# Kernel tuning notes

Hardware: AMD Instinct MI355X
Metric: run time of the kernel (lower is better)

## Reference

```python
import jax, jax.numpy as jnp
import numpy as np

# ---- fixed architecture constants (from init_kwargs) ----
N_WALL, N_ROOF, N_WINDOW = 4, 1, 2
N_RC = N_WALL + N_ROOF
HID = 32
ENC_LEN = 48
DT = 900.0
R_OPAQUE, C_OPAQUE = 10.0, 1.0e5
R_TRANS = 2.0
DIRECT_COEF, ABS_WALL_COEF, ABS_ROOF_COEF = 0.5, 0.5, 0.5
C_ZONE = 1.0e5
B, T = 2048, 1440


def setup_inputs() -> dict:
    key = jax.random.key(0)
    k0, k1, k2 = jax.random.split(key, 3)
    input_X = jax.random.normal(k0, (B, T, 7), dtype=jnp.float32)
    # EnvelopeRC deterministic inits
    rc_R_inv = jnp.concatenate([
        1.0 / (10.0 + 1.0 * jnp.arange(N_WALL, dtype=jnp.float32)),
        1.0 / (20.0 + 2.0 * jnp.arange(N_ROOF, dtype=jnp.float32))])
    rc_C_inv = jnp.concatenate([
        1.0 / (80.0 + 10.0 * jnp.arange(N_WALL, dtype=jnp.float32)),
        1.0 / (60.0 + 10.0 * jnp.arange(N_ROOF, dtype=jnp.float32))])
    window_R_inv = 1.0 / (1.0 + 0.1 * jnp.arange(N_WINDOW, dtype=jnp.float32))
    # Internal MLP: xavier_uniform with gain 0.1, zero bias
    lim1 = 0.1 * np.sqrt(6.0 / (2 + HID))
    int_W1 = jax.random.uniform(k1, (HID, 2), jnp.float32, -lim1, lim1)
    int_b1 = jnp.zeros((HID,), jnp.float32)
    lim2 = 0.1 * np.sqrt(6.0 / (HID + 1))
    int_W2 = jax.random.uniform(k2, (1, HID), jnp.float32, -lim2, lim2)
    int_b2 = jnp.zeros((1,), jnp.float32)
    return {
        'input_X': input_X,
        'rc_R_inv': rc_R_inv, 'rc_C_inv': rc_C_inv, 'window_R_inv': window_R_inv,
        'hvac_gain': jnp.float32(0.1),
        'int_W1': int_W1, 'int_b1': int_b1, 'int_W2': int_W2, 'int_b2': int_b2,
        'int_gain': jnp.float32(0.1),
        'direct_gain': jnp.float32(0.1), 'abs_wall': jnp.float32(0.1), 'abs_roof': jnp.float32(0.1),
        'zone_C_inv': jnp.float32(1.0 / 10000.0),
    }


def _forward(input_X, rc_R_inv, rc_C_inv, window_R_inv, hvac_gain,
             int_W1, int_b1, int_W2, int_b2, int_gain,
             direct_gain, abs_wall, abs_roof, zone_C_inv):
    sp = jax.nn.softplus
    Bn, Tn = input_X.shape[0], input_X.shape[1]
    tz_gt  = input_X[:, :, 0]   # [B,T]
    t_amb  = input_X[:, :, 1]
    sol    = input_X[:, :, 2]
    int_x  = input_X[:, :, 3:6]
    hvac_x = input_X[:, :, 6]

    # Internal MLP (state-free -> vectorized over time)
    h1  = jax.nn.relu(jnp.einsum('bti,hi->bth', int_x[:, :, :2], int_W1) + int_b1)
    sch = jax.nn.sigmoid(jnp.einsum('bth,oh->bto', h1, int_W2) + int_b2)[:, :, 0] + int_x[:, :, 2]
    q_int  = sp(int_gain) * 0.1 * sch          # [B,T]
    q_hvac = sp(hvac_gain) * 0.1 * hvac_x      # [B,T]

    # Bounded RC parameters
    r_inv   = sp(rc_R_inv) * (1.0 / R_OPAQUE)  # [n_rc]
    c_inv   = sp(rc_C_inv) * (1.0 / C_OPAQUE)  # [n_rc]
    win_rsum = jnp.sum(sp(window_R_inv)) * (1.0 / R_TRANS)
    abs_rc  = jnp.where(jnp.arange(N_RC) < N_WALL,
                        sp(abs_wall) * ABS_WALL_COEF,
                        sp(abs_roof) * ABS_ROOF_COEF)   # [n_rc]
    q_dir   = sp(direct_gain) * DIRECT_COEF * sol       # [B,T]
    cz_inv  = sp(zone_C_inv) * (1.0 / C_ZONE)

    # Initial state: Tmid_i = 0.7*Tzone0 + 0.3*Tamb0
    Tz0   = tz_gt[:, 0]                                      # [B]
    Tmid0 = jnp.broadcast_to((0.7 * Tz0 + 0.3 * t_amb[:, 0])[:, None], (Bn, N_RC))

    # Teacher forcing during encoder window: carry GT zone temp while t+1 < enc_len
    tz_gt_next = jnp.concatenate([tz_gt[:, 1:], tz_gt[:, -1:]], axis=1)  # [B,T]
    use_gt = (jnp.arange(Tn) + 1) < ENC_LEN                              # [T]

    xs = (t_amb.T, sol.T, q_dir.T, q_int.T, q_hvac.T, tz_gt_next.T, use_gt)

    def step(carry, x):
        Tz, Tmid = carry                      # [B], [B,n_rc]
        ta, so, qd, qi, qh, gt_next, ug = x
        q_in  = (ta[:, None] - Tmid) * r_inv
        q_out = (Tmid - Tz[:, None]) * r_inv
        dTmid = (q_in - q_out + so[:, None] * abs_rc) * c_inv
        q_env = jnp.sum(q_out, axis=1) + (ta - Tz) * win_rsum
        dTz   = (q_env + qi + qh + qd) * cz_inv
        Tz_new   = Tz + dTz * DT
        Tmid_new = Tmid + dTmid * DT
        Tz_carry = jnp.where(ug, gt_next, Tz_new)
        return (Tz_carry, Tmid_new), Tz_new

    _, tz_seq = jax.lax.scan(step, (Tz0, Tmid0), xs)   # [T,B]
    return jnp.transpose(tz_seq)[:, :, None]           # [B,T,1]


def reference(input_X, rc_R_inv, rc_C_inv, window_R_inv, hvac_gain,
              int_W1, int_b1, int_W2, int_b2, int_gain,
              direct_gain, abs_wall, abs_roof, zone_C_inv):
    return _forward(input_X, rc_R_inv, rc_C_inv, window_R_inv, hvac_gain,
                    int_W1, int_b1, int_W2, int_b2, int_gain,
                    direct_gain, abs_wall, abs_roof, zone_C_inv)
```

## Files before the change

kernel.cpp:

```cpp
#include <hip/hip_runtime.h>
#include <math.h>

#define BATCH 2048
#define TLEN  1440
#define CL0   48
#define CLS   12
#define NS    116
#define NCC   117
#define ER    128
#define TB    64
#define TT    48
#define LP    65

#define E_OFF    0
#define XC_OFF   (E_OFF + BATCH*ER*8)
#define A12_OFF  (XC_OFF + BATCH*NCC*8)
#define VCOL_OFF (A12_OFF + 64)
#define PRM_OFF  (VCOL_OFF + 96)
#define WS_FLOATS (PRM_OFF + 32)

__device__ __forceinline__ float sp_precise(float x) { return log1pf(expf(x)); }

__global__ void k0_params(const float* __restrict__ rcR, const float* __restrict__ rcC,
                          const float* __restrict__ winR, const float* __restrict__ hvg,
                          const float* __restrict__ ing, const float* __restrict__ dg,
                          const float* __restrict__ aw, const float* __restrict__ ar,
                          const float* __restrict__ zc, float* __restrict__ ws) {
  __shared__ float A0s[36], Ma[36], Mb[36], A4s[36], vbuf[2][8];
  int ln = threadIdx.x;
  float r[5], cc[5];
  #pragma unroll
  for (int j = 0; j < 5; ++j) { r[j] = sp_precise(rcR[j]) * 0.1f; cc[j] = sp_precise(rcC[j]) * 1e-5f; }
  float w    = (sp_precise(winR[0]) + sp_precise(winR[1])) * 0.5f;
  float cz   = sp_precise(zc[0]) * 1e-5f;
  float aW   = sp_precise(aw[0]) * 0.5f, aR = sp_precise(ar[0]) * 0.5f;
  float dtcz = 900.f * cz;
  if (ln == 0) {
    float* prm = ws + PRM_OFF;
    float rsum = 0.f;
    for (int j = 0; j < 5; ++j) {
      float P = 900.f * r[j] * cc[j];
      prm[j]      = P;
      prm[5 + j]  = 1.f - 2.f * P;
      prm[10 + j] = 900.f * cc[j] * ((j < 4) ? aW : aR);
      prm[15 + j] = dtcz * r[j];
      rsum += r[j];
    }
    prm[20] = 1.f - dtcz * (w + rsum);
    prm[21] = dtcz * w;
    prm[22] = dtcz;
    prm[23] = sp_precise(ing[0]) * 0.1f;
    prm[24] = sp_precise(hvg[0]) * 0.1f;
    prm[25] = sp_precise(dg[0])  * 0.5f;
    for (int i = 0; i < 36; ++i) A0s[i] = 0.f;
    A0s[0] = prm[20];
    for (int j = 0; j < 5; ++j) {
      A0s[0 * 6 + 1 + j]       = dtcz * r[j];
      A0s[(1 + j) * 6 + 0]     = prm[j];
      A0s[(1 + j) * 6 + 1 + j] = prm[5 + j];
    }
  }
  __syncthreads();
  int i6 = ln / 6, j6 = ln % 6;
  bool act = ln < 36;
#define MM(DST, L, R) { if (act) { float s = 0.f; \
  for (int m = 0; m < 6; ++m) s = fmaf((L)[i6 * 6 + m], (R)[m * 6 + j6], s); \
  (DST)[ln] = s; } __syncthreads(); }
  MM(Mb, A0s, A0s);
  MM(Ma, Mb, Mb);
  if (act) A4s[ln] = Ma[ln];
  __syncthreads();
  MM(Mb, Ma, Ma);
  MM(Ma, Mb, A4s);
  if (act) ws[A12_OFF + ln] = Ma[ln];
  if (ln < 6) vbuf[0][ln] = A0s[ln];
  __syncthreads();
  int cur = 0;
  for (int k = 0; k < CLS; ++k) {
    if (ln < 6) {
      ws[VCOL_OFF + ln * CLS + k] = vbuf[cur][ln];
      float s = 0.f;
      for (int m = 0; m < 6; ++m) s = fmaf(vbuf[cur][m], A0s[m * 6 + ln], s);
      vbuf[1 - cur][ln] = s;
    }
    __syncthreads();
    cur ^= 1;
  }
}

__global__ __launch_bounds__(256) void k2a_scan(const float* __restrict__ X,
    const float* __restrict__ W1, const float* __restrict__ B1,
    const float* __restrict__ W2, const float* __restrict__ B2,
    float* __restrict__ out, float* __restrict__ ws) {
  __shared__ float sTa[TT * LP], sSo[TT * LP], sU[TT * LP], sTz[TT * LP];
  int tile   = blockIdx.x;
  int tile_t = tile >> 5;
  int tile_b = tile & 31;
  int t0 = tile_t * TT, b0 = tile_b * TB;
  const float* prm = ws + PRM_OFF;
  float P0 = prm[0], P1 = prm[1], P2 = prm[2], P3 = prm[3], P4 = prm[4];
  float M0 = prm[5], M1 = prm[6], M2 = prm[7], M3 = prm[8], M4 = prm[9];
  float Q0 = prm[10], Q1 = prm[11], Q2 = prm[12], Q3 = prm[13], Q4 = prm[14];
  float K0 = prm[15], K1 = prm[16], K2 = prm[17], K3 = prm[18], K4 = prm[19];
  float AZ = prm[20];
  float dtczw = prm[21], dtcz = prm[22], cInt = prm[23], cHv = prm[24], cDir = prm[25];
  float b2v = B2[0];

  #pragma unroll 4
  for (int r = 0; r < (TB * TT) / 256; ++r) {
    int e  = threadIdx.x + 256 * r;
    int bl = e / TT;
    int tt = e - bl * TT;
    const float* x = X + ((size_t)(b0 + bl) * TLEN + (t0 + tt)) * 7;
    float x0 = x[0], ta = x[1], so = x[2], x3 = x[3], x4 = x[4], x5 = x[5], hv = x[6];
    float acc = b2v;
    #pragma unroll
    for (int h = 0; h < 32; ++h) {
      float z = fmaf(W1[2 * h], x3, fmaf(W1[2 * h + 1], x4, B1[h]));
      acc = fmaf(W2[h], fmaxf(z, 0.f), acc);
    }
    float sch = __frcp_rn(1.f + __expf(-acc)) + x5;
    float q = fmaf(cInt, sch, fmaf(cHv, hv, cDir * so));
    float u = fmaf(dtczw, ta, dtcz * q);
    sTa[tt * LP + bl] = ta;
    sSo[tt * LP + bl] = so;
    sU [tt * LP + bl] = u;
    sTz[tt * LP + bl] = x0;
  }
  __syncthreads();

  int w = threadIdx.x >> 6, l = threadIdx.x & 63;
  int b = b0 + l;
  bool tile0 = (tile_t == 0);
  int c, kbeg, ksteps;
  if (tile0) { c = 0; kbeg = 0; ksteps = (w == 0) ? CL0 : 0; }
  else       { c = 1 + (tile_t - 1) * 4 + w; kbeg = w * CLS; ksteps = CLS; }
  float Tz = 0.f, T0 = 0.f, T1 = 0.f, T2 = 0.f, T3 = 0.f, T4 = 0.f;
  if (tile0) {
    float tz0 = sTz[l], ta0 = sTa[l];
    Tz = tz0;
    float tm = fmaf(0.7f, tz0, 0.3f * ta0);
    T0 = T1 = T2 = T3 = T4 = tm;
  }
  for (int k = kbeg; k < kbeg + ksteps; ++k) {
    float ta = sTa[k * LP + l], so = sSo[k * LP + l], u = sU[k * LP + l];
    float d = fmaf(K0, T0, u);
    d = fmaf(K1, T1, d); d = fmaf(K2, T2, d); d = fmaf(K3, T3, d); d = fmaf(K4, T4, d);
    float tzn = fmaf(AZ, Tz, d);
    T0 = fmaf(M0, T0, fmaf(P0, Tz, fmaf(P0, ta, Q0 * so)));
    T1 = fmaf(M1, T1, fmaf(P1, Tz, fmaf(P1, ta, Q1 * so)));
    T2 = fmaf(M2, T2, fmaf(P2, Tz, fmaf(P2, ta, Q2 * so)));
    T3 = fmaf(M3, T3, fmaf(P3, Tz, fmaf(P3, ta, Q3 * so)));
    T4 = fmaf(M4, T4, fmaf(P4, Tz, fmaf(P4, ta, Q4 * so)));
    float nz = tzn;
    if (tile0 && k < 47) nz = sTz[(k + 1) * LP + l];
    sTz[k * LP + l] = tzn;
    Tz = nz;
  }
  if (ksteps > 0) {
    float* ep = ws + E_OFF + ((size_t)b * ER + c) * 8;
    *(float4*)ep       = make_float4(Tz, T0, T1, T2);
    *(float2*)(ep + 4) = make_float2(T3, T4);
  }
  __syncthreads();

  #pragma unroll
  for (int r = 0; r < 3; ++r) {
    int f  = threadIdx.x + 256 * r;
    int bl = f / 12, t4 = f - bl * 12;
    float4 v = make_float4(sTz[(4 * t4 + 0) * LP + bl], sTz[(4 * t4 + 1) * LP + bl],
                           sTz[(4 * t4 + 2) * LP + bl], sTz[(4 * t4 + 3) * LP + bl]);
    *(float4*)(out + (size_t)(b0 + bl) * TLEN + t0 + 4 * t4) = v;
  }
}

__global__ __launch_bounds__(256) void k2s_combine(const float* __restrict__ e,
                                                   float* __restrict__ xc,
                                                   const float* __restrict__ A12) {
  __shared__ float sAp[7][40];
  int ln = threadIdx.x;
  if (ln < 36) sAp[0][ln] = A12[ln];
  __syncthreads();
  int i6 = ln / 6, j6 = ln % 6;
  bool act = ln < 36;
  for (int k = 1; k < 7; ++k) {
    if (act) {
      float s = 0.f;
      #pragma unroll
      for (int m = 0; m < 6; ++m) s = fmaf(sAp[k - 1][i6 * 6 + m], sAp[k - 1][m * 6 + j6], s);
      sAp[k][ln] = s;
    }
    __syncthreads();
  }
  int w = ln >> 6, l = ln & 63;
  int b = blockIdx.x * 4 + w;
  const float* pA = e + ((size_t)b * ER + l) * 8;
  const float* pB = e + ((size_t)b * ER + 64 + l) * 8;
  float yA[6], yB[6];
  { float4 q = *(const float4*)pA; float2 r = *(const float2*)(pA + 4);
    yA[0] = q.x; yA[1] = q.y; yA[2] = q.z; yA[3] = q.w; yA[4] = r.x; yA[5] = r.y; }
  { float4 q = *(const float4*)pB; float2 r = *(const float2*)(pB + 4);
    yB[0] = q.x; yB[1] = q.y; yB[2] = q.z; yB[3] = q.w; yB[4] = r.x; yB[5] = r.y; }
  #pragma unroll
  for (int k = 0; k < 6; ++k) {
    int d = 1 << k;
    int src = (l - d) & 63;
    float tA[6], tB[6];
    #pragma unroll
    for (int j = 0; j < 6; ++j) { tA[j] = __shfl(yA[j], src); tB[j] = __shfl(yB[j], src); }
    bool up = (l >= d);
    float sA[6], sB[6];
    #pragma unroll
    for (int j = 0; j < 6; ++j) { sA[j] = up ? tA[j] : 0.f; sB[j] = up ? tB[j] : tA[j]; }
    float nA[6], nB[6];
    #pragma unroll
    for (int i = 0; i < 6; ++i) {
      float uA = yA[i], uB = yB[i];
      #pragma unroll
      for (int m = 0; m < 6; ++m) {
        float a = sAp[k][i * 6 + m];
        uA = fmaf(a, sA[m], uA);
        uB = fmaf(a, sB[m], uB);
      }
      nA[i] = uA; nB[i] = uB;
    }
    #pragma unroll
    for (int i = 0; i < 6; ++i) { yA[i] = nA[i]; yB[i] = nB[i]; }
  }
  #pragma unroll
  for (int i = 0; i < 6; ++i) {
    float uB = yB[i];
    #pragma unroll
    for (int m = 0; m < 6; ++m) uB = fmaf(sAp[6][i * 6 + m], yA[m], uB);
    yB[i] = uB;
  }
  {
    float* xp = xc + ((size_t)b * NCC + (l + 1)) * 8;
    *(float4*)xp       = make_float4(yA[0], yA[1], yA[2], yA[3]);
    *(float2*)(xp + 4) = make_float2(yA[4], yA[5]);
  }
  if (l < 52) {
    float* xp = xc + ((size_t)b * NCC + (65 + l)) * 8;
    *(float4*)xp       = make_float4(yB[0], yB[1], yB[2], yB[3]);
    *(float2*)(xp + 4) = make_float2(yB[4], yB[5]);
  }
}

__global__ __launch_bounds__(256) void k2c_correct(float* __restrict__ out,
                                                   const float* __restrict__ ws) {
  __shared__ float V[6 * CLS];
  for (int i = threadIdx.x; i < 6 * CLS; i += 256) V[i] = ws[VCOL_OFF + i];
  __syncthreads();
  int tid = blockIdx.x * 256 + threadIdx.x;
  int b   = tid / ((TLEN - CL0) / 4);
  int u   = tid - b * ((TLEN - CL0) / 4);
  int tt0 = u * 4;
  int c   = tt0 / CLS + 1;
  int kk0 = tt0 - (c - 1) * CLS;
  const float* xp = ws + XC_OFF + ((size_t)b * NCC + c) * 8;
  float s0 = xp[0], s1 = xp[1], s2 = xp[2], s3 = xp[3], s4 = xp[4], s5 = xp[5];
  float4* op = (float4*)(out + (size_t)b * TLEN + CL0 + tt0);
  float4 v = *op;
  float acc[4] = {v.x, v.y, v.z, v.w};
  #pragma unroll
  for (int ee = 0; ee < 4; ++ee) {
    int kk = kk0 + ee;
    float s = acc[ee];
    s = fmaf(V[0 * CLS + kk], s0, s);
    s = fmaf(V[1 * CLS + kk], s1, s);
    s = fmaf(V[2 * CLS + kk], s2, s);
    s = fmaf(V[3 * CLS + kk], s3, s);
    s = fmaf(V[4 * CLS + kk], s4, s);
    s = fmaf(V[5 * CLS + kk], s5, s);
    acc[ee] = s;
  }
  *op = make_float4(acc[0], acc[1], acc[2], acc[3]);
}

__global__ void k_fallback(const float* __restrict__ X,
    const float* __restrict__ rcR, const float* __restrict__ rcC,
    const float* __restrict__ winR, const float* __restrict__ hvg,
    const float* __restrict__ W1, const float* __restrict__ B1,
    const float* __restrict__ W2, const float* __restrict__ B2,
    const float* __restrict__ ing, const float* __restrict__ dg,
    const float* __restrict__ aw, const float* __restrict__ ar,
    const float* __restrict__ zc, float* __restrict__ out) {
  int b = blockIdx.x * 64 + threadIdx.x;
  if (b >= BATCH) return;
  float r[5], cc[5], P[5], M[5], Q[5], K[5];
  float rsum = 0.f;
  for (int j = 0; j < 5; ++j) { r[j] = sp_precise(rcR[j]) * 0.1f; cc[j] = sp_precise(rcC[j]) * 1e-5f; rsum += r[j]; }
  float w = (sp_precise(winR[0]) + sp_precise(winR[1])) * 0.5f;
  float cz = sp_precise(zc[0]) * 1e-5f;
  float aW = sp_precise(aw[0]) * 0.5f, aR = sp_precise(ar[0]) * 0.5f;
  float dtcz = 900.f * cz;
  for (int j = 0; j < 5; ++j) {
    P[j] = 900.f * r[j] * cc[j]; M[j] = 1.f - 2.f * P[j];
    Q[j] = 900.f * cc[j] * ((j < 4) ? aW : aR); K[j] = dtcz * r[j];
  }
  float AZ = 1.f - dtcz * (w + rsum), dtczw = dtcz * w;
  float cInt = sp_precise(ing[0]) * 0.1f, cHv = sp_precise(hvg[0]) * 0.1f, cDir = sp_precise(dg[0]) * 0.5f;
  const float* xb = X + (size_t)b * (TLEN * 7);
  float Tz = xb[0];
  float tm = fmaf(0.7f, xb[0], 0.3f * xb[1]);
  float Tm[5] = {tm, tm, tm, tm, tm};
  for (int t = 0; t < TLEN; ++t) {
    const float* x = xb + t * 7;
    float ta = x[1], so = x[2], x3 = x[3], x4 = x[4], x5 = x[5], hv = x[6];
    float acc = B2[0];
    #pragma unroll
    for (int h = 0; h < 32; ++h) {
      float z = fmaf(W1[2 * h], x3, fmaf(W1[2 * h + 1], x4, B1[h]));
      acc = fmaf(W2[h], fmaxf(z, 0.f), acc);
    }
    float sch = __frcp_rn(1.f + __expf(-acc)) + x5;
    float q = fmaf(cInt, sch, fmaf(cHv, hv, cDir * so));
    float u = fmaf(dtczw, ta, dtcz * q);
    float d = u;
    #pragma unroll
    for (int j = 0; j < 5; ++j) d = fmaf(K[j], Tm[j], d);
    float tzn = fmaf(AZ, Tz, d);
    #pragma unroll
    for (int j = 0; j < 5; ++j)
      Tm[j] = fmaf(M[j], Tm[j], fmaf(P[j], Tz, fmaf(P[j], ta, Q[j] * so)));
    out[(size_t)b * TLEN + t] = tzn;
    Tz = (t < 47) ? x[7] : tzn;
  }
}

extern "C" void kernel_launch(void* const* d_in, const int* in_sizes, int n_in,
                              void* d_out, int out_size, void* d_ws, size_t ws_size,
                              hipStream_t stream) {
  const float* X    = (const float*)d_in[0];
  const float* rcR  = (const float*)d_in[1];
  const float* rcC  = (const float*)d_in[2];
  const float* winR = (const float*)d_in[3];
  const float* hvg  = (const float*)d_in[4];
  const float* W1   = (const float*)d_in[5];
  const float* B1   = (const float*)d_in[6];
  const float* W2   = (const float*)d_in[7];
  const float* B2   = (const float*)d_in[8];
  const float* ing  = (const float*)d_in[9];
  const float* dg   = (const float*)d_in[10];
  const float* aw   = (const float*)d_in[11];
  const float* ar   = (const float*)d_in[12];
  const float* zc   = (const float*)d_in[13];
  float* out = (float*)d_out;
  float* ws  = (float*)d_ws;

  if (ws_size >= (size_t)WS_FLOATS * sizeof(float)) {
    k0_params<<<1, 64, 0, stream>>>(rcR, rcC, winR, hvg, ing, dg, aw, ar, zc, ws);
    k2a_scan<<<(BATCH / TB) * (TLEN / TT), 256, 0, stream>>>(X, W1, B1, W2, B2, out, ws);
    k2s_combine<<<BATCH / 4, 256, 0, stream>>>(ws + E_OFF, ws + XC_OFF, ws + A12_OFF);
    k2c_correct<<<(BATCH * (TLEN - CL0)) / (256 * 4), 256, 0, stream>>>(out, ws);
  } else {
    k_fallback<<<BATCH / 64, 64, 0, stream>>>(X, rcR, rcC, winR, hvg, W1, B1, W2, B2,
                                              ing, dg, aw, ar, zc, out);
  }
}
```

Baseline: 183.6 us.

## Fuse param setup into scan kernels and merge combine with correction

Drops the single-block parameter kernel: every scan block and every combine block now recomputes the softplus-derived coefficients itself. The chunk-carry combine and the output correction are merged into one kernel with one block per batch row. Carries stay in shared memory instead of round-tripping through a global workspace, so two launches and a global buffer go away. The cost is redundant per-block transcendental work and 6x6 matrix-power setup in each of 2048 blocks, and only 64 of 256 threads do the scan phase.

```diff
diff --git a/kernel.cpp b/kernel.cpp
--- a/kernel.cpp
+++ b/kernel.cpp
@@ -13,97 +13,68 @@
 #define LP    65
 
 #define E_OFF    0
-#define XC_OFF   (E_OFF + BATCH*ER*8)
-#define A12_OFF  (XC_OFF + BATCH*NCC*8)
-#define VCOL_OFF (A12_OFF + 64)
-#define PRM_OFF  (VCOL_OFF + 96)
-#define WS_FLOATS (PRM_OFF + 32)
+#define WS_FLOATS (E_OFF + BATCH*ER*8)
 
 __device__ __forceinline__ float sp_precise(float x) { return log1pf(expf(x)); }
 
-__global__ void k0_params(const float* __restrict__ rcR, const float* __restrict__ rcC,
-                          const float* __restrict__ winR, const float* __restrict__ hvg,
-                          const float* __restrict__ ing, const float* __restrict__ dg,
-                          const float* __restrict__ aw, const float* __restrict__ ar,
-                          const float* __restrict__ zc, float* __restrict__ ws) {
-  __shared__ float A0s[36], Ma[36], Mb[36], A4s[36], vbuf[2][8];
-  int ln = threadIdx.x;
+struct Prm {
+  float P[5], M[5], Q[5], K[5];
+  float AZ, dtczw, dtcz, cInt, cHv, cDir;
   float r[5], cc[5];
+};
+__device__ __forceinline__ Prm make_prm(
+    const float* __restrict__ rcR, const float* __restrict__ rcC,
+    const float* __restrict__ winR, const float* __restrict__ hvg,
+    const float* __restrict__ ing, const float* __restrict__ dg,
+    const float* __restrict__ aw, const float* __restrict__ ar,
+    const float* __restrict__ zc) {
+  Prm p;
   #pragma unroll
-  for (int j = 0; j < 5; ++j) { r[j] = sp_precise(rcR[j]) * 0.1f; cc[j] = sp_precise(rcC[j]) * 1e-5f; }
-  float w    = (sp_precise(winR[0]) + sp_precise(winR[1])) * 0.5f;
-  float cz   = sp_precise(zc[0]) * 1e-5f;
-  float aW   = sp_precise(aw[0]) * 0.5f, aR = sp_precise(ar[0]) * 0.5f;
+  for (int j = 0; j < 5; ++j) { p.r[j] = sp_precise(rcR[j]) * 0.1f; p.cc[j] = sp_precise(rcC[j]) * 1e-5f; }
+  float w  = (sp_precise(winR[0]) + sp_precise(winR[1])) * 0.5f;
+  float cz = sp_precise(zc[0]) * 1e-5f;
+  float aW = sp_precise(aw[0]) * 0.5f, aR = sp_precise(ar[0]) * 0.5f;
   float dtcz = 900.f * cz;
-  if (ln == 0) {
-    float* prm = ws + PRM_OFF;
-    float rsum = 0.f;
-    for (int j = 0; j < 5; ++j) {
-      float P = 900.f * r[j] * cc[j];
-      prm[j]      = P;
-      prm[5 + j]  = 1.f - 2.f * P;
-      prm[10 + j] = 900.f * cc[j] * ((j < 4) ? aW : aR);
-      prm[15 + j] = dtcz * r[j];
-      rsum += r[j];
-    }
-    prm[20] = 1.f - dtcz * (w + rsum);
-    prm[21] = dtcz * w;
-    prm[22] = dtcz;
-    prm[23] = sp_precise(ing[0]) * 0.1f;
-    prm[24] = sp_precise(hvg[0]) * 0.1f;
-    prm[25] = sp_precise(dg[0])  * 0.5f;
-    for (int i = 0; i < 36; ++i) A0s[i] = 0.f;
-    A0s[0] = prm[20];
-    for (int j = 0; j < 5; ++j) {
-      A0s[0 * 6 + 1 + j]       = dtcz * r[j];
-      A0s[(1 + j) * 6 + 0]     = prm[j];
-      A0s[(1 + j) * 6 + 1 + j] = prm[5 + j];
-    }
-  }
-  __syncthreads();
-  int i6 = ln / 6, j6 = ln % 6;
-  bool act = ln < 36;
-#define MM(DST, L, R) { if (act) { float s = 0.f; \
-  for (int m = 0; m < 6; ++m) s = fmaf((L)[i6 * 6 + m], (R)[m * 6 + j6], s); \
-  (DST)[ln] = s; } __syncthreads(); }
-  MM(Mb, A0s, A0s);
-  MM(Ma, Mb, Mb);
-  if (act) A4s[ln] = Ma[ln];
-  __syncthreads();
-  MM(Mb, Ma, Ma);
-  MM(Ma, Mb, A4s);
-  if (act) ws[A12_OFF + ln] = Ma[ln];
-  if (ln < 6) vbuf[0][ln] = A0s[ln];
-  __syncthreads();
-  int cur = 0;
-  for (int k = 0; k < CLS; ++k) {
-    if (ln < 6) {
-      ws[VCOL_OFF + ln * CLS + k] = vbuf[cur][ln];
-      float s = 0.f;
-      for (int m = 0; m < 6; ++m) s = fmaf(vbuf[cur][m], A0s[m * 6 + ln], s);
-      vbuf[1 - cur][ln] = s;
-    }
-    __syncthreads();
-    cur ^= 1;
-  }
+  float rsum = 0.f;
+  #pragma unroll
+  for (int j = 0; j < 5; ++j) {
+    float P = 900.f * p.r[j] * p.cc[j];
+    p.P[j] = P;
+    p.M[j] = 1.f - 2.f * P;
+    p.Q[j] = 900.f * p.cc[j] * ((j < 4) ? aW : aR);
+    p.K[j] = dtcz * p.r[j];
+    rsum += p.r[j];
+  }
+  p.AZ    = 1.f - dtcz * (w + rsum);
+  p.dtczw = dtcz * w;
+  p.dtcz  = dtcz;
+  p.cInt  = sp_precise(ing[0]) * 0.1f;
+  p.cHv   = sp_precise(hvg[0]) * 0.1f;
+  p.cDir  = sp_precise(dg[0])  * 0.5f;
+  return p;
 }
 
 __global__ __launch_bounds__(256) void k2a_scan(const float* __restrict__ X,
+    const float* __restrict__ rcR, const float* __restrict__ rcC,
+    const float* __restrict__ winR, const float* __restrict__ hvg,
     const float* __restrict__ W1, const float* __restrict__ B1,
     const float* __restrict__ W2, const float* __restrict__ B2,
+    const float* __restrict__ ing, const float* __restrict__ dg,
+    const float* __restrict__ aw, const float* __restrict__ ar,
+    const float* __restrict__ zc,
     float* __restrict__ out, float* __restrict__ ws) {
   __shared__ float sTa[TT * LP], sSo[TT * LP], sU[TT * LP], sTz[TT * LP];
   int tile   = blockIdx.x;
   int tile_t = tile >> 5;
   int tile_b = tile & 31;
   int t0 = tile_t * TT, b0 = tile_b * TB;
-  const float* prm = ws + PRM_OFF;
-  float P0 = prm[0], P1 = prm[1], P2 = prm[2], P3 = prm[3], P4 = prm[4];
-  float M0 = prm[5], M1 = prm[6], M2 = prm[7], M3 = prm[8], M4 = prm[9];
-  float Q0 = prm[10], Q1 = prm[11], Q2 = prm[12], Q3 = prm[13], Q4 = prm[14];
-  float K0 = prm[15], K1 = prm[16], K2 = prm[17], K3 = prm[18], K4 = prm[19];
-  float AZ = prm[20];
-  float dtczw = prm[21], dtcz = prm[22], cInt = prm[23], cHv = prm[24], cDir = prm[25];
+  Prm pp = make_prm(rcR, rcC, winR, hvg, ing, dg, aw, ar, zc);
+  float P0 = pp.P[0], P1 = pp.P[1], P2 = pp.P[2], P3 = pp.P[3], P4 = pp.P[4];
+  float M0 = pp.M[0], M1 = pp.M[1], M2 = pp.M[2], M3 = pp.M[3], M4 = pp.M[4];
+  float Q0 = pp.Q[0], Q1 = pp.Q[1], Q2 = pp.Q[2], Q3 = pp.Q[3], Q4 = pp.Q[4];
+  float K0 = pp.K[0], K1 = pp.K[1], K2 = pp.K[2], K3 = pp.K[3], K4 = pp.K[4];
+  float AZ = pp.AZ, dtczw = pp.dtczw, dtcz = pp.dtcz;
+  float cInt = pp.cInt, cHv = pp.cHv, cDir = pp.cDir;
   float b2v = B2[0];
 
   #pragma unroll 4
@@ -174,15 +145,44 @@
   }
 }
 
-__global__ __launch_bounds__(256) void k2s_combine(const float* __restrict__ e,
-                                                   float* __restrict__ xc,
-                                                   const float* __restrict__ A12) {
+__global__ __launch_bounds__(256) void k2sc(
+    const float* __restrict__ rcR, const float* __restrict__ rcC,
+    const float* __restrict__ winR, const float* __restrict__ hvg,
+    const float* __restrict__ ing, const float* __restrict__ dg,
+    const float* __restrict__ aw, const float* __restrict__ ar,
+    const float* __restrict__ zc,
+    const float* __restrict__ e, float* __restrict__ out) {
+  __shared__ float A0s[36], Ma[36], Mb[36], A4s[36], vbuf[2][8];
   __shared__ float sAp[7][40];
+  __shared__ float sV[6 * CLS];
+  __shared__ float sXC[NCC][6];
   int ln = threadIdx.x;
-  if (ln < 36) sAp[0][ln] = A12[ln];
+  Prm pp = make_prm(rcR, rcC, winR, hvg, ing, dg, aw, ar, zc);
+  if (ln == 0) {
+    #pragma unroll
+    for (int i = 0; i < 36; ++i) A0s[i] = 0.f;
+    A0s[0] = pp.AZ;
+    #pragma unroll
+    for (int j = 0; j < 5; ++j) {
+      A0s[0 * 6 + 1 + j]       = pp.dtcz * pp.r[j];
+      A0s[(1 + j) * 6 + 0]     = pp.P[j];
+      A0s[(1 + j) * 6 + 1 + j] = pp.M[j];
+    }
+  }
   __syncthreads();
   int i6 = ln / 6, j6 = ln % 6;
   bool act = ln < 36;
+#define MM(DST, L, R) { if (act) { float s = 0.f; \
+  for (int m = 0; m < 6; ++m) s = fmaf((L)[i6 * 6 + m], (R)[m * 6 + j6], s); \
+  (DST)[ln] = s; } __syncthreads(); }
+  MM(Mb, A0s, A0s);
+  MM(Ma, Mb, Mb);
+  if (act) A4s[ln] = Ma[ln];
+  __syncthreads();
+  MM(Mb, Ma, Ma);
+  MM(Ma, Mb, A4s);
+  if (act) sAp[0][ln] = Ma[ln];
+  __syncthreads();
   for (int k = 1; k < 7; ++k) {
     if (act) {
       float s = 0.f;
@@ -192,89 +192,96 @@
     }
     __syncthreads();
   }
-  int w = ln >> 6, l = ln & 63;
-  int b = blockIdx.x * 4 + w;
-  const float* pA = e + ((size_t)b * ER + l) * 8;
-  const float* pB = e + ((size_t)b * ER + 64 + l) * 8;
-  float yA[6], yB[6];
-  { float4 q = *(const float4*)pA; float2 r = *(const float2*)(pA + 4);
-    yA[0] = q.x; yA[1] = q.y; yA[2] = q.z; yA[3] = q.w; yA[4] = r.x; yA[5] = r.y; }
-  { float4 q = *(const float4*)pB; float2 r = *(const float2*)(pB + 4);
-    yB[0] = q.x; yB[1] = q.y; yB[2] = q.z; yB[3] = q.w; yB[4] = r.x; yB[5] = r.y; }
-  #pragma unroll
-  for (int k = 0; k < 6; ++k) {
-    int d = 1 << k;
-    int src = (l - d) & 63;
-    float tA[6], tB[6];
-    #pragma unroll
-    for (int j = 0; j < 6; ++j) { tA[j] = __shfl(yA[j], src); tB[j] = __shfl(yB[j], src); }
-    bool up = (l >= d);
-    float sA[6], sB[6];
-    #pragma unroll
-    for (int j = 0; j < 6; ++j) { sA[j] = up ? tA[j] : 0.f; sB[j] = up ? tB[j] : tA[j]; }
-    float nA[6], nB[6];
+  if (ln < 6) vbuf[0][ln] = A0s[ln];
+  __syncthreads();
+  int cur = 0;
+  for (int k = 0; k < CLS; ++k) {
+    if (ln < 6) {
+      sV[ln * CLS + k] = vbuf[cur][ln];
+      float s = 0.f;
+      #pragma unroll
+      for (int m = 0; m < 6; ++m) s = fmaf(vbuf[cur][m], A0s[m * 6 + ln], s);
+      vbuf[1 - cur][ln] = s;
+    }
+    __syncthreads();
+    cur ^= 1;
+  }
+
+  int b = blockIdx.x;
+  if (ln < 64) {
+    int l = ln;
+    const float* pA = e + ((size_t)b * ER + l) * 8;
+    const float* pB = e + ((size_t)b * ER + 64 + l) * 8;
+    float yA[6], yB[6];
+    { float4 q = *(const float4*)pA; float2 r = *(const float2*)(pA + 4);
+      yA[0] = q.x; yA[1] = q.y; yA[2] = q.z; yA[3] = q.w; yA[4] = r.x; yA[5] = r.y; }
+    { float4 q = *(const float4*)pB; float2 r = *(const float2*)(pB + 4);
+      yB[0] = q.x; yB[1] = q.y; yB[2] = q.z; yB[3] = q.w; yB[4] = r.x; yB[5] = r.y; }
+    #pragma unroll
+    for (int k = 0; k < 6; ++k) {
+      int d = 1 << k;
+      int src = (l - d) & 63;
+      float tA[6], tB[6];
+      #pragma unroll
+      for (int j = 0; j < 6; ++j) { tA[j] = __shfl(yA[j], src); tB[j] = __shfl(yB[j], src); }
+      bool up = (l >= d);
+      float sA[6], sB[6];
+      #pragma unroll
+      for (int j = 0; j < 6; ++j) { sA[j] = up ? tA[j] : 0.f; sB[j] = up ? tB[j] : tA[j]; }
+      float nA[6], nB[6];
+      #pragma unroll
+      for (int i = 0; i < 6; ++i) {
+        float uA = yA[i], uB = yB[i];
+        #pragma unroll
+        for (int m = 0; m < 6; ++m) {
+          float a = sAp[k][i * 6 + m];
+          uA = fmaf(a, sA[m], uA);
+          uB = fmaf(a, sB[m], uB);
+        }
+        nA[i] = uA; nB[i] = uB;
+      }
+      #pragma unroll
+      for (int i = 0; i < 6; ++i) { yA[i] = nA[i]; yB[i] = nB[i]; }
+    }
     #pragma unroll
     for (int i = 0; i < 6; ++i) {
-      float uA = yA[i], uB = yB[i];
-      #pragma unroll
-      for (int m = 0; m < 6; ++m) {
-        float a = sAp[k][i * 6 + m];
-        uA = fmaf(a, sA[m], uA);
-        uB = fmaf(a, sB[m], uB);
-      }
-      nA[i] = uA; nB[i] = uB;
-    }
-    #pragma unroll
-    for (int i = 0; i < 6; ++i) { yA[i] = nA[i]; yB[i] = nB[i]; }
-  }
-  #pragma unroll
-  for (int i = 0; i < 6; ++i) {
-    float uB = yB[i];
-    #pragma unroll
-    for (int m = 0; m < 6; ++m) uB = fmaf(sAp[6][i * 6 + m], yA[m], uB);
-    yB[i] = uB;
-  }
-  {
-    float* xp = xc + ((size_t)b * NCC + (l + 1)) * 8;
-    *(float4*)xp       = make_float4(yA[0], yA[1], yA[2], yA[3]);
-    *(float2*)(xp + 4) = make_float2(yA[4], yA[5]);
-  }
-  if (l < 52) {
-    float* xp = xc + ((size_t)b * NCC + (65 + l)) * 8;
-    *(float4*)xp       = make_float4(yB[0], yB[1], yB[2], yB[3]);
-    *(float2*)(xp + 4) = make_float2(yB[4], yB[5]);
-  }
-}
-
-__global__ __launch_bounds__(256) void k2c_correct(float* __restrict__ out,
-                                                   const float* __restrict__ ws) {
-  __shared__ float V[6 * CLS];
-  for (int i = threadIdx.x; i < 6 * CLS; i += 256) V[i] = ws[VCOL_OFF + i];
-  __syncthreads();
-  int tid = blockIdx.x * 256 + threadIdx.x;
-  int b   = tid / ((TLEN - CL0) / 4);
-  int u   = tid - b * ((TLEN - CL0) / 4);
-  int tt0 = u * 4;
-  int c   = tt0 / CLS + 1;
-  int kk0 = tt0 - (c - 1) * CLS;
-  const float* xp = ws + XC_OFF + ((size_t)b * NCC + c) * 8;
-  float s0 = xp[0], s1 = xp[1], s2 = xp[2], s3 = xp[3], s4 = xp[4], s5 = xp[5];
-  float4* op = (float4*)(out + (size_t)b * TLEN + CL0 + tt0);
-  float4 v = *op;
-  float acc[4] = {v.x, v.y, v.z, v.w};
-  #pragma unroll
-  for (int ee = 0; ee < 4; ++ee) {
-    int kk = kk0 + ee;
-    float s = acc[ee];
-    s = fmaf(V[0 * CLS + kk], s0, s);
-    s = fmaf(V[1 * CLS + kk], s1, s);
-    s = fmaf(V[2 * CLS + kk], s2, s);
-    s = fmaf(V[3 * CLS + kk], s3, s);
-    s = fmaf(V[4 * CLS + kk], s4, s);
-    s = fmaf(V[5 * CLS + kk], s5, s);
-    acc[ee] = s;
-  }
-  *op = make_float4(acc[0], acc[1], acc[2], acc[3]);
+      float uB = yB[i];
+      #pragma unroll
+      for (int m = 0; m < 6; ++m) uB = fmaf(sAp[6][i * 6 + m], yA[m], uB);
+      yB[i] = uB;
+    }
+    #pragma unroll
+    for (int j = 0; j < 6; ++j) sXC[l + 1][j] = yA[j];
+    if (l < 52) {
+      #pragma unroll
+      for (int j = 0; j < 6; ++j) sXC[65 + l][j] = yB[j];
+    }
+  }
+  __syncthreads();
+
+  for (int q = ln; q < (TLEN - CL0) / 4; q += 256) {
+    int tt0 = q * 4;
+    int c   = tt0 / CLS + 1;
+    int kk0 = tt0 - (c - 1) * CLS;
+    float s0 = sXC[c][0], s1 = sXC[c][1], s2 = sXC[c][2];
+    float s3 = sXC[c][3], s4 = sXC[c][4], s5 = sXC[c][5];
+    float4* op = (float4*)(out + (size_t)b * TLEN + CL0 + tt0);
+    float4 v = *op;
+    float acc[4] = {v.x, v.y, v.z, v.w};
+    #pragma unroll
+    for (int ee = 0; ee < 4; ++ee) {
+      int kk = kk0 + ee;
+      float s = acc[ee];
+      s = fmaf(sV[0 * CLS + kk], s0, s);
+      s = fmaf(sV[1 * CLS + kk], s1, s);
+      s = fmaf(sV[2 * CLS + kk], s2, s);
+      s = fmaf(sV[3 * CLS + kk], s3, s);
+      s = fmaf(sV[4 * CLS + kk], s4, s);
+      s = fmaf(sV[5 * CLS + kk], s5, s);
+      acc[ee] = s;
+    }
+    *op = make_float4(acc[0], acc[1], acc[2], acc[3]);
+  }
 }
 
 __global__ void k_fallback(const float* __restrict__ X,
@@ -287,19 +294,7 @@
     const float* __restrict__ zc, float* __restrict__ out) {
   int b = blockIdx.x * 64 + threadIdx.x;
   if (b >= BATCH) return;
-  float r[5], cc[5], P[5], M[5], Q[5], K[5];
-  float rsum = 0.f;
-  for (int j = 0; j < 5; ++j) { r[j] = sp_precise(rcR[j]) * 0.1f; cc[j] = sp_precise(rcC[j]) * 1e-5f; rsum += r[j]; }
-  float w = (sp_precise(winR[0]) + sp_precise(winR[1])) * 0.5f;
-  float cz = sp_precise(zc[0]) * 1e-5f;
-  float aW = sp_precise(aw[0]) * 0.5f, aR = sp_precise(ar[0]) * 0.5f;
-  float dtcz = 900.f * cz;
-  for (int j = 0; j < 5; ++j) {
-    P[j] = 900.f * r[j] * cc[j]; M[j] = 1.f - 2.f * P[j];
-    Q[j] = 900.f * cc[j] * ((j < 4) ? aW : aR); K[j] = dtcz * r[j];
-  }
-  float AZ = 1.f - dtcz * (w + rsum), dtczw = dtcz * w;
-  float cInt = sp_precise(ing[0]) * 0.1f, cHv = sp_precise(hvg[0]) * 0.1f, cDir = sp_precise(dg[0]) * 0.5f;
+  Prm pp = make_prm(rcR, rcC, winR, hvg, ing, dg, aw, ar, zc);
   const float* xb = X + (size_t)b * (TLEN * 7);
   float Tz = xb[0];
   float tm = fmaf(0.7f, xb[0], 0.3f * xb[1]);
@@ -314,15 +309,15 @@
       acc = fmaf(W2[h], fmaxf(z, 0.f), acc);
     }
     float sch = __frcp_rn(1.f + __expf(-acc)) + x5;
-    float q = fmaf(cInt, sch, fmaf(cHv, hv, cDir * so));
-    float u = fmaf(dtczw, ta, dtcz * q);
+    float q = fmaf(pp.cInt, sch, fmaf(pp.cHv, hv, pp.cDir * so));
+    float u = fmaf(pp.dtczw, ta, pp.dtcz * q);
     float d = u;
     #pragma unroll
-    for (int j = 0; j < 5; ++j) d = fmaf(K[j], Tm[j], d);
-    float tzn = fmaf(AZ, Tz, d);
+    for (int j = 0; j < 5; ++j) d = fmaf(pp.K[j], Tm[j], d);
+    float tzn = fmaf(pp.AZ, Tz, d);
     #pragma unroll
     for (int j = 0; j < 5; ++j)
-      Tm[j] = fmaf(M[j], Tm[j], fmaf(P[j], Tz, fmaf(P[j], ta, Q[j] * so)));
+      Tm[j] = fmaf(pp.M[j], Tm[j], fmaf(pp.P[j], Tz, fmaf(pp.P[j], ta, pp.Q[j] * so)));
     out[(size_t)b * TLEN + t] = tzn;
     Tz = (t < 47) ? x[7] : tzn;
   }
@@ -349,10 +344,10 @@
   float* ws  = (float*)d_ws;
 
   if (ws_size >= (size_t)WS_FLOATS * sizeof(float)) {
-    k0_params<<<1, 64, 0, stream>>>(rcR, rcC, winR, hvg, ing, dg, aw, ar, zc, ws);
-    k2a_scan<<<(BATCH / TB) * (TLEN / TT), 256, 0, stream>>>(X, W1, B1, W2, B2, out, ws);
-    k2s_combine<<<BATCH / 4, 256, 0, stream>>>(ws + E_OFF, ws + XC_OFF, ws + A12_OFF);
-    k2c_correct<<<(BATCH * (TLEN - CL0)) / (256 * 4), 256, 0, stream>>>(out, ws);
+    k2a_scan<<<(BATCH / TB) * (TLEN / TT), 256, 0, stream>>>(
+        X, rcR, rcC, winR, hvg, W1, B1, W2, B2, ing, dg, aw, ar, zc, out, ws);
+    k2sc<<<BATCH, 256, 0, stream>>>(
+        rcR, rcC, winR, hvg, ing, dg, aw, ar, zc, ws + E_OFF, out);
   } else {
     k_fallback<<<BATCH / 64, 64, 0, stream>>>(X, rcR, rcC, winR, hvg, W1, B1, W2, B2,
                                               ing, dg, aw, ar, zc, out);
```

Measured after the change: 196.3 us. 6.9% more time.

## Fuse chunk-state combine and output correction into one per-batch kernel

Applied to the files above, without the earlier changes.

Merges the prefix-combine kernel and the correction kernel into a single kernel with one block per batch row. The combined chunk states stay in shared memory instead of round-tripping through a global workspace array. The matrix powers A^(12·2^k) are now computed once in the parameter kernel rather than in every combine block. The trade-off is that only one wavefront per block does the shuffle scan while the other three wait, and the kernel launches 2048 smaller blocks.

```diff
diff --git a/kernel.cpp b/kernel.cpp
--- a/kernel.cpp
+++ b/kernel.cpp
@@ -13,9 +13,8 @@
 #define LP    65
 
 #define E_OFF    0
-#define XC_OFF   (E_OFF + BATCH*ER*8)
-#define A12_OFF  (XC_OFF + BATCH*NCC*8)
-#define VCOL_OFF (A12_OFF + 64)
+#define AP_OFF   (E_OFF + BATCH*ER*8)
+#define VCOL_OFF (AP_OFF + 280)
 #define PRM_OFF  (VCOL_OFF + 96)
 #define WS_FLOATS (PRM_OFF + 32)
 
@@ -72,7 +71,19 @@
   __syncthreads();
   MM(Mb, Ma, Ma);
   MM(Ma, Mb, A4s);
-  if (act) ws[A12_OFF + ln] = Ma[ln];
+  if (act) ws[AP_OFF + 0 * 40 + ln] = Ma[ln];
+  MM(Mb, Ma, Ma);
+  if (act) ws[AP_OFF + 1 * 40 + ln] = Mb[ln];
+  MM(Ma, Mb, Mb);
+  if (act) ws[AP_OFF + 2 * 40 + ln] = Ma[ln];
+  MM(Mb, Ma, Ma);
+  if (act) ws[AP_OFF + 3 * 40 + ln] = Mb[ln];
+  MM(Ma, Mb, Mb);
+  if (act) ws[AP_OFF + 4 * 40 + ln] = Ma[ln];
+  MM(Mb, Ma, Ma);
+  if (act) ws[AP_OFF + 5 * 40 + ln] = Mb[ln];
+  MM(Ma, Mb, Mb);
+  if (act) ws[AP_OFF + 6 * 40 + ln] = Ma[ln];
   if (ln < 6) vbuf[0][ln] = A0s[ln];
   __syncthreads();
   int cur = 0;
@@ -174,107 +185,92 @@
   }
 }
 
-__global__ __launch_bounds__(256) void k2s_combine(const float* __restrict__ e,
-                                                   float* __restrict__ xc,
-                                                   const float* __restrict__ A12) {
+__global__ __launch_bounds__(256) void k2sc(const float* __restrict__ e,
+                                            float* __restrict__ out,
+                                            const float* __restrict__ ws) {
   __shared__ float sAp[7][40];
+  __shared__ float sV[6 * CLS];
+  __shared__ float sXC[NCC][6];
   int ln = threadIdx.x;
-  if (ln < 36) sAp[0][ln] = A12[ln];
-  __syncthreads();
-  int i6 = ln / 6, j6 = ln % 6;
-  bool act = ln < 36;
-  for (int k = 1; k < 7; ++k) {
-    if (act) {
-      float s = 0.f;
-      #pragma unroll
-      for (int m = 0; m < 6; ++m) s = fmaf(sAp[k - 1][i6 * 6 + m], sAp[k - 1][m * 6 + j6], s);
-      sAp[k][ln] = s;
-    }
-    __syncthreads();
-  }
-  int w = ln >> 6, l = ln & 63;
-  int b = blockIdx.x * 4 + w;
-  const float* pA = e + ((size_t)b * ER + l) * 8;
-  const float* pB = e + ((size_t)b * ER + 64 + l) * 8;
-  float yA[6], yB[6];
-  { float4 q = *(const float4*)pA; float2 r = *(const float2*)(pA + 4);
-    yA[0] = q.x; yA[1] = q.y; yA[2] = q.z; yA[3] = q.w; yA[4] = r.x; yA[5] = r.y; }
-  { float4 q = *(const float4*)pB; float2 r = *(const float2*)(pB + 4);
-    yB[0] = q.x; yB[1] = q.y; yB[2] = q.z; yB[3] = q.w; yB[4] = r.x; yB[5] = r.y; }
-  #pragma unroll
-  for (int k = 0; k < 6; ++k) {
-    int d = 1 << k;
-    int src = (l - d) & 63;
-    float tA[6], tB[6];
-    #pragma unroll
-    for (int j = 0; j < 6; ++j) { tA[j] = __shfl(yA[j], src); tB[j] = __shfl(yB[j], src); }
-    bool up = (l >= d);
-    float sA[6], sB[6];
-    #pragma unroll
-    for (int j = 0; j < 6; ++j) { sA[j] = up ? tA[j] : 0.f; sB[j] = up ? tB[j] : tA[j]; }
-    float nA[6], nB[6];
+  for (int i = ln; i < 7 * 40; i += 256) sAp[0][i] = ws[AP_OFF + i];
+  for (int i = ln; i < 6 * CLS; i += 256) sV[i] = ws[VCOL_OFF + i];
+  __syncthreads();
+
+  int b = blockIdx.x;
+  if (ln < 64) {
+    int l = ln;
+    const float* pA = e + ((size_t)b * ER + l) * 8;
+    const float* pB = e + ((size_t)b * ER + 64 + l) * 8;
+    float yA[6], yB[6];
+    { float4 q = *(const float4*)pA; float2 r = *(const float2*)(pA + 4);
+      yA[0] = q.x; yA[1] = q.y; yA[2] = q.z; yA[3] = q.w; yA[4] = r.x; yA[5] = r.y; }
+    { float4 q = *(const float4*)pB; float2 r = *(const float2*)(pB + 4);
+      yB[0] = q.x; yB[1] = q.y; yB[2] = q.z; yB[3] = q.w; yB[4] = r.x; yB[5] = r.y; }
+    #pragma unroll
+    for (int k = 0; k < 6; ++k) {
+      int d = 1 << k;
+      int src = (l - d) & 63;
+      float tA[6], tB[6];
+      #pragma unroll
+      for (int j = 0; j < 6; ++j) { tA[j] = __shfl(yA[j], src); tB[j] = __shfl(yB[j], src); }
+      bool up = (l >= d);
+      float sA[6], sB[6];
+      #pragma unroll
+      for (int j = 0; j < 6; ++j) { sA[j] = up ? tA[j] : 0.f; sB[j] = up ? tB[j] : tA[j]; }
+      float nA[6], nB[6];
+      #pragma unroll
+      for (int i = 0; i < 6; ++i) {
+        float uA = yA[i], uB = yB[i];
+        #pragma unroll
+        for (int m = 0; m < 6; ++m) {
+          float a = sAp[k][i * 6 + m];
+          uA = fmaf(a, sA[m], uA);
+          uB = fmaf(a, sB[m], uB);
+        }
+        nA[i] = uA; nB[i] = uB;
+      }
+      #pragma unroll
+      for (int i = 0; i < 6; ++i) { yA[i] = nA[i]; yB[i] = nB[i]; }
+    }
     #pragma unroll
     for (int i = 0; i < 6; ++i) {
-      float uA = yA[i], uB = yB[i];
-      #pragma unroll
-      for (int m = 0; m < 6; ++m) {
-        float a = sAp[k][i * 6 + m];
-        uA = fmaf(a, sA[m], uA);
-        uB = fmaf(a, sB[m], uB);
-      }
-      nA[i] = uA; nB[i] = uB;
-    }
-    #pragma unroll
-    for (int i = 0; i < 6; ++i) { yA[i] = nA[i]; yB[i] = nB[i]; }
-  }
-  #pragma unroll
-  for (int i = 0; i < 6; ++i) {
-    float uB = yB[i];
-    #pragma unroll
-    for (int m = 0; m < 6; ++m) uB = fmaf(sAp[6][i * 6 + m], yA[m], uB);
-    yB[i] = uB;
-  }
-  {
-    float* xp = xc + ((size_t)b * NCC + (l + 1)) * 8;
-    *(float4*)xp       = make_float4(yA[0], yA[1], yA[2], yA[3]);
-    *(float2*)(xp + 4) = make_float2(yA[4], yA[5]);
-  }
-  if (l < 52) {
-    float* xp = xc + ((size_t)b * NCC + (65 + l)) * 8;
-    *(float4*)xp       = make_float4(yB[0], yB[1], yB[2], yB[3]);
-    *(float2*)(xp + 4) = make_float2(yB[4], yB[5]);
-  }
-}
-
-__global__ __launch_bounds__(256) void k2c_correct(float* __restrict__ out,
-                                                   const float* __restrict__ ws) {
-  __shared__ float V[6 * CLS];
-  for (int i = threadIdx.x; i < 6 * CLS; i += 256) V[i] = ws[VCOL_OFF + i];
-  __syncthreads();
-  int tid = blockIdx.x * 256 + threadIdx.x;
-  int b   = tid / ((TLEN - CL0) / 4);
-  int u   = tid - b * ((TLEN - CL0) / 4);
-  int tt0 = u * 4;
-  int c   = tt0 / CLS + 1;
-  int kk0 = tt0 - (c - 1) * CLS;
-  const float* xp = ws + XC_OFF + ((size_t)b * NCC + c) * 8;
-  float s0 = xp[0], s1 = xp[1], s2 = xp[2], s3 = xp[3], s4 = xp[4], s5 = xp[5];
-  float4* op = (float4*)(out + (size_t)b * TLEN + CL0 + tt0);
-  float4 v = *op;
-  float acc[4] = {v.x, v.y, v.z, v.w};
-  #pragma unroll
-  for (int ee = 0; ee < 4; ++ee) {
-    int kk = kk0 + ee;
-    float s = acc[ee];
-    s = fmaf(V[0 * CLS + kk], s0, s);
-    s = fmaf(V[1 * CLS + kk], s1, s);
-    s = fmaf(V[2 * CLS + kk], s2, s);
-    s = fmaf(V[3 * CLS + kk], s3, s);
-    s = fmaf(V[4 * CLS + kk], s4, s);
-    s = fmaf(V[5 * CLS + kk], s5, s);
-    acc[ee] = s;
-  }
-  *op = make_float4(acc[0], acc[1], acc[2], acc[3]);
+      float uB = yB[i];
+      #pragma unroll
+      for (int m = 0; m < 6; ++m) uB = fmaf(sAp[6][i * 6 + m], yA[m], uB);
+      yB[i] = uB;
+    }
+    #pragma unroll
+    for (int j = 0; j < 6; ++j) sXC[l + 1][j] = yA[j];
+    if (l < 52) {
+      #pragma unroll
+      for (int j = 0; j < 6; ++j) sXC[65 + l][j] = yB[j];
+    }
+  }
+  __syncthreads();
+
+  for (int q = ln; q < (TLEN - CL0) / 4; q += 256) {
+    int tt0 = q * 4;
+    int c   = tt0 / CLS + 1;
+    int kk0 = tt0 - (c - 1) * CLS;
+    float s0 = sXC[c][0], s1 = sXC[c][1], s2 = sXC[c][2];
+    float s3 = sXC[c][3], s4 = sXC[c][4], s5 = sXC[c][5];
+    float4* op = (float4*)(out + (size_t)b * TLEN + CL0 + tt0);
+    float4 v = *op;
+    float acc[4] = {v.x, v.y, v.z, v.w};
+    #pragma unroll
+    for (int ee = 0; ee < 4; ++ee) {
+      int kk = kk0 + ee;
+      float s = acc[ee];
+      s = fmaf(sV[0 * CLS + kk], s0, s);
+      s = fmaf(sV[1 * CLS + kk], s1, s);
+      s = fmaf(sV[2 * CLS + kk], s2, s);
+      s = fmaf(sV[3 * CLS + kk], s3, s);
+      s = fmaf(sV[4 * CLS + kk], s4, s);
+      s = fmaf(sV[5 * CLS + kk], s5, s);
+      acc[ee] = s;
+    }
+    *op = make_float4(acc[0], acc[1], acc[2], acc[3]);
+  }
 }
 
 __global__ void k_fallback(const float* __restrict__ X,
@@ -351,8 +347,7 @@
   if (ws_size >= (size_t)WS_FLOATS * sizeof(float)) {
     k0_params<<<1, 64, 0, stream>>>(rcR, rcC, winR, hvg, ing, dg, aw, ar, zc, ws);
     k2a_scan<<<(BATCH / TB) * (TLEN / TT), 256, 0, stream>>>(X, W1, B1, W2, B2, out, ws);
-    k2s_combine<<<BATCH / 4, 256, 0, stream>>>(ws + E_OFF, ws + XC_OFF, ws + A12_OFF);
-    k2c_correct<<<(BATCH * (TLEN - CL0)) / (256 * 4), 256, 0, stream>>>(out, ws);
+    k2sc<<<BATCH, 256, 0, stream>>>(ws + E_OFF, out, ws);
   } else {
     k_fallback<<<BATCH / 64, 64, 0, stream>>>(X, rcR, rcC, winR, hvg, W1, B1, W2, B2,
                                               ing, dg, aw, ar, zc, out);
```

Result: no change. 181.9 us, median of 2 (-0.9%).
